# Performance work log

Hardware: AMD Instinct MI355X
Metric: run time of the kernel (lower is better)

Reference implementation:

```python
import jax, jax.numpy as jnp
import numpy as np

BATCH, SEQ, D_DIM, H = 8, 4096, 256, 64


def _log_step_init(u, dmin=0.001, dmax=0.1):
    lg_dmin, lg_dmax = np.log(dmin), np.log(dmax)
    return u * (lg_dmax - lg_dmin) + lg_dmin


def _make_hippo_nplr(N):
    q = np.arange(N)
    hip = np.sqrt((2 * q[:, None] + 1) * (2 * q[None, :] + 1))
    hip = np.where(q[:, None] > q[None, :], hip, 0.0) + np.diag(q + 1.0)
    hip = -hip
    p = np.sqrt(q + 0.5)
    S = hip + np.outer(p, p)  # NPLR: A = S - p p^T
    lam, V = np.linalg.eig(S)
    P = V.conj().T @ p
    B = V.conj().T @ (np.sqrt(2.0) * p)
    return lam.astype(np.complex64), P.astype(np.complex64), B.astype(np.complex64)


def _ri(z):
    return np.stack([z.real, z.imag], axis=-1).astype(np.float32)


def _cx(p):
    return p[..., 0] + 1j * p[..., 1]


def setup_inputs() -> dict:
    key = jax.random.key(0)
    k1, k2, k3 = jax.random.split(key, 3)
    lam, P, B = _make_hippo_nplr(H)
    lam_ri = jnp.asarray(_ri(lam))                      # (H, 2)
    P_ri = jnp.asarray(_ri(P))                          # (H, 2)
    B_ri = jnp.asarray(np.tile(_ri(B)[None], (D_DIM, 1, 1)))  # (D, H, 2)
    C_ri = jax.random.uniform(k1, (D_DIM, H, 2), dtype=jnp.float32)  # torch.rand complex
    Dp = jnp.ones((1, 1, D_DIM), dtype=jnp.float32)
    log_delta = jnp.asarray(
        _log_step_init(np.asarray(jax.random.uniform(k2, (D_DIM,), dtype=jnp.float32)))
    ).astype(jnp.float32)
    x = jax.random.normal(k3, (BATCH, SEQ, D_DIM), dtype=jnp.float32)
    return {"x": x, "lam_ri": lam_ri, "P_ri": P_ri, "B_ri": B_ri,
            "C_ri": C_ri, "D": Dp, "log_delta": log_delta}


def reference(x, lam_ri, P_ri, B_ri, C_ri, D, log_delta):
    # S4 DPLR generating-function kernel via Woodbury / Cauchy dot-products + iFFT conv.
    lam, P, B, C = _cx(lam_ri), _cx(P_ri), _cx(B_ri), _cx(C_ri)  # (H,), (H,), (D,H), (D,H)
    delta = jnp.exp(log_delta)                                   # (D,)
    L = x.shape[1]
    z = jnp.exp(2j * jnp.pi * jnp.arange(L) / L).astype(jnp.complex64)  # roots of unity (L,)
    coef = 2.0 / (1.0 + z)                                        # (L,)
    g = (2.0 * (1.0 - z) / (1.0 + z))[None, :] / delta[:, None].astype(jnp.complex64)  # (D, L)
    cauchy = 1.0 / (g[:, :, None] - lam[None, None, :])           # (D, L, H) -- R(z) diagonal
    # Woodbury: C (R - R P P* R / (1 + P* R P)) B  as 4 Cauchy dot products
    k00 = jnp.einsum("dh,dlh->dl", C * B, cauchy)
    k01 = jnp.einsum("dh,dlh->dl", C * P[None, :], cauchy)
    k10 = jnp.einsum("dh,dlh->dl", P.conj()[None, :] * B, cauchy)
    k11 = jnp.einsum("h,dlh->dl", P.conj() * P, cauchy)
    at_roots = coef[None, :] * (k00 - k01 * k10 / (1.0 + k11))    # (D, L)
    K = jnp.fft.ifft(at_roots, axis=-1).real.astype(x.dtype)      # (D, L) time-domain kernel
    # circular convolution along the sequence axis, per channel
    Xf = jnp.fft.fft(x, axis=1)                                   # (B, L, D)
    Kf = jnp.fft.fft(K, axis=-1)                                  # (D, L)
    y = jnp.fft.ifft(Xf * Kf.T[None, :, :], axis=1).real.astype(x.dtype)
    return y + D * x
```

## Files before the change

kernel.cpp:

```cpp
#include <hip/hip_runtime.h>
#include <math.h>

#ifndef M_PI
#define M_PI 3.14159265358979323846
#endif

#define BB 8
#define LL 4096
#define DD 256
#define HH 64

__device__ __forceinline__ float2 cmulf(float2 a, float2 b) {
    return make_float2(a.x*b.x - a.y*b.y, a.x*b.y + a.y*b.x);
}
__device__ __forceinline__ float2 cmul_cs(float2 a, float c, float s) {
    return make_float2(a.x*c - a.y*s, a.x*s + a.y*c);
}
__device__ __forceinline__ float2 cadd(float2 a, float2 b){return make_float2(a.x+b.x, a.y+b.y);}
__device__ __forceinline__ float2 csub(float2 a, float2 b){return make_float2(a.x-b.x, a.y-b.y);}

#define DR4(i) ((((i)&3)<<2)|((i)>>2))
#define SPW(k) ((((k)>>4)*17) + ((k)&15))

template<int SGN>
__device__ __forceinline__ void r4(float2& a, float2& b, float2& c, float2& d) {
    float2 e0 = cadd(a, c), e1 = csub(a, c);
    float2 o0 = cadd(b, d), o1 = csub(b, d);
    float2 j1 = (SGN < 0) ? make_float2(o1.y, -o1.x) : make_float2(-o1.y, o1.x);
    a = cadd(e0, o0);
    b = cadd(e1, j1);
    c = csub(e0, o0);
    d = csub(e1, j1);
}

template<int SGN>
__device__ __forceinline__ void fft16(float2 v[16]) {
    const float C16[10] = {1.f, 0.92387953f, 0.70710678f, 0.38268343f, 0.f,
                           -0.38268343f, -0.70710678f, -0.92387953f, -1.f, -0.92387953f};
    const float S16[10] = {0.f, 0.38268343f, 0.70710678f, 0.92387953f, 1.f,
                           0.92387953f, 0.70710678f, 0.38268343f, 0.f, -0.38268343f};
#pragma unroll
    for (int a0 = 0; a0 < 4; ++a0)
        r4<SGN>(v[a0], v[a0+4], v[a0+8], v[a0+12]);
#pragma unroll
    for (int a0 = 1; a0 < 4; ++a0) {
#pragma unroll
        for (int j0 = 1; j0 < 4; ++j0) {
            const int e = a0*j0;
            const float cc = C16[e];
            const float ss = (SGN < 0) ? -S16[e] : S16[e];
            v[a0 + 4*j0] = cmul_cs(v[a0 + 4*j0], cc, ss);
        }
    }
#pragma unroll
    for (int j0 = 0; j0 < 4; ++j0)
        r4<SGN>(v[4*j0+0], v[4*j0+1], v[4*j0+2], v[4*j0+3]);
}

__device__ __forceinline__ float2 woodbury_coef(
    float k00r, float k00i, float k01r, float k01i,
    float k10r, float k10i, float k11r, float k11i, float tc)
{
    float wr = 1.f + k11r, wi = k11i;
    float winv = __builtin_amdgcn_rcpf(wr*wr + wi*wi);
    float qr = k01r*k10r - k01i*k10i;
    float qi = k01r*k10i + k01i*k10r;
    float dr = (qr*wr + qi*wi) * winv;
    float di = (qi*wr - qr*wi) * winv;
    float rr = k00r - dr, ri = k00i - di;
    return make_float2(rr - tc*ri, tc*rr + ri);
}

__global__ __launch_bounds__(256)
void s4_cauchy_kf(const float* __restrict__ lam_ri,
                  const float* __restrict__ P_ri,
                  const float* __restrict__ B_ri,
                  const float* __restrict__ C_ri,
                  const float* __restrict__ Dp,
                  const float* __restrict__ log_delta,
                  float2* __restrict__ Kf)
{
    __shared__ float4 WA[HH];
    __shared__ float4 WB[HH];
    __shared__ float  WC[HH];
    const int d   = blockIdx.y;
    const int tid = threadIdx.x;
    if (tid < HH) {
        const int h = tid;
        float br = B_ri[(d*HH + h)*2 + 0], bi = B_ri[(d*HH + h)*2 + 1];
        float cr = C_ri[(d*HH + h)*2 + 0], ci = C_ri[(d*HH + h)*2 + 1];
        float pr = P_ri[h*2 + 0], pi = P_ri[h*2 + 1];
        WA[h] = make_float4(cr*br - ci*bi, cr*bi + ci*br,
                            cr*pr - ci*pi, cr*pi + ci*pr);
        WB[h] = make_float4(pr*br + pi*bi, pr*bi - pi*br,
                            pr*pr + pi*pi, -lam_ri[h*2+0]);
        WC[h] = lam_ri[h*2+1];
    }
    __syncthreads();
    const int t0 = blockIdx.x * blockDim.x + tid;
    const float delta = expf(log_delta[d]);
    const float dterm = Dp[d];
    const float SCALE = 0.5f / 4096.f;

    const int l1 = t0;
    const int l2 = t0 + 1024;

    float sn1, cs1, sn2, cs2;
    sincosf((float)l1 * (float)(M_PI/4096.0), &sn1, &cs1);
    sincosf((float)l2 * (float)(M_PI/4096.0), &sn2, &cs2);
    const float invd = __builtin_amdgcn_rcpf(delta);
    const float tt1 = sn1 * __builtin_amdgcn_rcpf(cs1);
    const float tt2 = sn2 * __builtin_amdgcn_rcpf(cs2);
    const float G1 = -2.f * tt1 * invd;
    const float G2 = -2.f * tt2 * invd;

    float a00r1=0,a00i1=0,a01r1=0,a01i1=0,a10r1=0,a10i1=0,a11r1=0,a11i1=0;
    float b00r1=0,b00i1=0,b01r1=0,b01i1=0;
    float a00r2=0,a00i2=0,a01r2=0,a01i2=0,a10r2=0,a10i2=0,a11r2=0,a11i2=0;
    float b00r2=0,b00i2=0,b01r2=0,b01i2=0;
    float sr2048 = 0.f;

#pragma unroll 4
    for (int h = 0; h < HH; ++h) {
        const float4 wa = WA[h];
        const float4 wb = WB[h];
        const float  li = WC[h];
        const float  nr  = wb.w;
        const float  nr2 = nr*nr;
        sr2048 += wa.x;
        {
            const float nip = G1 - li, nim = G1 + li;
            const float dp = fmaf(nip, nip, nr2);
            const float dm = fmaf(nim, nim, nr2);
            const float ip = __builtin_amdgcn_rcpf(dp*dm);
            const float invp = dm*ip, invm = dp*ip;
            const float rrp = nr*invp, rip = -nip*invp;
            const float rrm = nr*invm, rim =  nim*invm;
            a00r1 += wa.x*rrp - wa.y*rip;  a00i1 += wa.x*rip + wa.y*rrp;
            a01r1 += wa.z*rrp - wa.w*rip;  a01i1 += wa.z*rip + wa.w*rrp;
            a10r1 += wb.x*rrp - wb.y*rip;  a10i1 += wb.x*rip + wb.y*rrp;
            a11r1 += wb.z*rrp;             a11i1 += wb.z*rip;
            b00r1 += wa.x*rrm - wa.y*rim;  b00i1 += wa.x*rim + wa.y*rrm;
            b01r1 += wa.z*rrm - wa.w*rim;  b01i1 += wa.z*rim + wa.w*rrm;
        }
        {
            const float nip = G2 - li, nim = G2 + li;
            const float dp = fmaf(nip, nip, nr2);
            const float dm = fmaf(nim, nim, nr2);
            const float ip = __builtin_amdgcn_rcpf(dp*dm);
            const float invp = dm*ip, invm = dp*ip;
            const float rrp = nr*invp, rip = -nip*invp;
            const float rrm = nr*invm, rim =  nim*invm;
            a00r2 += wa.x*rrp - wa.y*rip;  a00i2 += wa.x*rip + wa.y*rrp;
            a01r2 += wa.z*rrp - wa.w*rip;  a01i2 += wa.z*rip + wa.w*rrp;
            a10r2 += wb.x*rrp - wb.y*rip;  a10i2 += wb.x*rip + wb.y*rrp;
            a11r2 += wb.z*rrp;             a11i2 += wb.z*rip;
            b00r2 += wa.x*rrm - wa.y*rim;  b00i2 += wa.x*rim + wa.y*rrm;
            b01r2 += wa.z*rrm - wa.w*rim;  b01i2 += wa.z*rim + wa.w*rrm;
        }
    }

    {
        float2 ar1 = woodbury_coef(a00r1,a00i1,a01r1,a01i1,a10r1,a10i1,a11r1,a11i1, -tt1);
        float2 ar2 = woodbury_coef(b00r1,b00i1,b01r1,b01i1,a10r1,-a10i1,a11r1,-a11i1, +tt1);
        float2 kf = make_float2((0.5f*(ar1.x + ar2.x) + dterm)*SCALE,
                                (0.5f*(ar1.y - ar2.y))*SCALE);
        Kf[(size_t)d*LL + l1] = kf;
    }
    {
        float2 ar1 = woodbury_coef(a00r2,a00i2,a01r2,a01i2,a10r2,a10i2,a11r2,a11i2, -tt2);
        float2 ar2 = woodbury_coef(b00r2,b00i2,b01r2,b01i2,a10r2,-a10i2,a11r2,-a11i2, +tt2);
        float2 kf = make_float2((0.5f*(ar1.x + ar2.x) + dterm)*SCALE,
                                (0.5f*(ar1.y - ar2.y))*SCALE);
        Kf[(size_t)d*LL + l2] = kf;
    }
    if (t0 == 0) {
        Kf[(size_t)d*LL + 2048] = make_float2((0.5f*delta*sr2048 + dterm)*SCALE, 0.f);
    }
}

__global__ __launch_bounds__(256)
void s4_fftconv(const float* __restrict__ x, const float2* __restrict__ Kf,
                float* __restrict__ y)
{
    __shared__ float2 As[4352];
    const int tid = threadIdx.x;
    const int p  = ((blockIdx.x & 7) << 7) | (blockIdx.x >> 3);
    const int b  = p >> 7;
    const int d2 = p & 127;

    const float2* xp = (const float2*)x + ((size_t)b*LL)*(DD/2) + d2;
    float2*       yp = (float2*)y       + ((size_t)b*LL)*(DD/2) + d2;
    const float2* Keb = Kf + (size_t)(2*d2)  *LL;
    const float2* Kob = Kf + (size_t)(2*d2+1)*LL;

    float2 v[16];

    {
        const int r = tid;
#pragma unroll
        for (int a = 0; a < 16; ++a)
            v[a] = xp[(size_t)(a*256 + r)*(DD/2)];
    }
    float2 pKe[9], pKo[9];
#pragma unroll
    for (int i = 0; i < 9; ++i) {
        int k = tid + (i << 8); if (k > 2048) k = 2048;
        pKe[i] = Keb[k];
        pKo[i] = Kob[k];
    }

    {
        const int r = tid;
        fft16<-1>(v);
        float2 base; sincosf(-(float)(2.0*M_PI/4096.0)*(float)r, &base.y, &base.x);
        float2 w = make_float2(1.f, 0.f);
#pragma unroll
        for (int k0 = 0; k0 < 16; ++k0) {
            As[17*r + k0] = cmulf(v[DR4(k0)], w);
            w = cmulf(w, base);
        }
    }
    __syncthreads();

    {
        const int k0 = tid >> 4, c = tid & 15;
#pragma unroll
        for (int bb = 0; bb < 16; ++bb)
            v[bb] = As[272*bb + 17*c + k0];
        __syncthreads();
        fft16<-1>(v);
        float2 base; sincosf(-(float)(2.0*M_PI/256.0)*(float)c, &base.y, &base.x);
        float2 w = make_float2(1.f, 0.f);
#pragma unroll
        for (int m0 = 0; m0 < 16; ++m0) {
            As[272*k0 + 17*c + m0] = cmulf(v[DR4(m0)], w);
            w = cmulf(w, base);
        }
    }
    __syncthreads();

    {
        const int k0 = tid >> 4, m0 = tid & 15;
#pragma unroll
        for (int c = 0; c < 16; ++c)
            v[c] = As[272*k0 + 17*c + m0];
        __syncthreads();
        fft16<-1>(v);
        const int s17 = 17*m0 + k0;
#pragma unroll
        for (int m1 = 0; m1 < 16; ++m1)
            As[s17 + 272*m1] = v[DR4(m1)];
    }
    __syncthreads();

    {
#pragma unroll
        for (int i = 0; i < 9; ++i) {
            int k = tid + (i << 8);
            if (k <= 2048) {
                int mk = (4096 - k) & 4095;
                float2 Zk = As[SPW(k)];
                float2 Zm = As[SPW(mk)];
                float2 Ke = pKe[i];
                float2 Ko = pKo[i];
                float2 S  = make_float2(Ke.x + Ko.x, Ke.y + Ko.y);
                float2 Df = make_float2(Ke.x - Ko.x, Ke.y - Ko.y);
                float2 cZm = make_float2(Zm.x, -Zm.y);
                float2 t0 = cmulf(Zk,  S);
                float2 t1 = cmulf(cZm, Df);
                float2 t2 = cmulf(cZm, S);
                float2 t3 = cmulf(Zk,  Df);
                As[SPW(k)]  = make_float2(t0.x + t1.x,   t0.y + t1.y);
                As[SPW(mk)] = make_float2(t2.x + t3.x, -(t2.y + t3.y));
            }
        }
    }
    __syncthreads();

    {
        const int k0 = tid >> 4, m0 = tid & 15;
        const int s17 = 17*m0 + k0;
#pragma unroll
        for (int m1 = 0; m1 < 16; ++m1)
            v[m1] = As[s17 + 272*m1];
        __syncthreads();
        fft16<1>(v);
        float2 base; sincosf((float)(2.0*M_PI/256.0)*(float)m0, &base.y, &base.x);
        float2 w = make_float2(1.f, 0.f);
#pragma unroll
        for (int c = 0; c < 16; ++c) {
            As[272*k0 + 17*c + m0] = cmulf(v[DR4(c)], w);
            w = cmulf(w, base);
        }
    }
    __syncthreads();

    {
        const int k0 = tid >> 4, c = tid & 15;
#pragma unroll
        for (int m0 = 0; m0 < 16; ++m0)
            v[m0] = As[272*k0 + 17*c + m0];
        __syncthreads();
        fft16<1>(v);
        float2 w, st;
        sincosf((float)(2.0*M_PI/4096.0)*(float)(c*k0), &w.y, &w.x);
        sincosf((float)(2.0*M_PI/256.0)*(float)k0,      &st.y, &st.x);
#pragma unroll
        for (int bb = 0; bb < 16; ++bb) {
            As[272*bb + 17*c + k0] = cmulf(v[DR4(bb)], w);
            w = cmulf(w, st);
        }
    }
    __syncthreads();

    {
        const int r = tid;
#pragma unroll
        for (int k0 = 0; k0 < 16; ++k0)
            v[k0] = As[17*r + k0];
        fft16<1>(v);
#pragma unroll
        for (int a = 0; a < 16; ++a)
            yp[(size_t)(a*256 + r)*(DD/2)] = v[DR4(a)];
    }
}

extern "C" void kernel_launch(void* const* d_in, const int* in_sizes, int n_in,
                              void* d_out, int out_size, void* d_ws, size_t ws_size,
                              hipStream_t stream)
{
    (void)in_sizes; (void)n_in; (void)out_size; (void)ws_size;
    const float* x         = (const float*)d_in[0];
    const float* lam_ri    = (const float*)d_in[1];
    const float* P_ri      = (const float*)d_in[2];
    const float* B_ri      = (const float*)d_in[3];
    const float* C_ri      = (const float*)d_in[4];
    const float* Dp        = (const float*)d_in[5];
    const float* log_delta = (const float*)d_in[6];
    float* y = (float*)d_out;

    float2* Kf = (float2*)d_ws;

    s4_cauchy_kf<<<dim3(4, DD), 256, 0, stream>>>(lam_ri, P_ri, B_ri, C_ri, Dp, log_delta, Kf);
    s4_fftconv<<<dim3(BB*DD/2), 256, 0, stream>>>(x, Kf, y);
}
```

Before: 163.9 us.

## Process four channels per block with float4 IO and XOR-swizzled shared memory

```diff
diff --git a/kernel.cpp b/kernel.cpp
--- a/kernel.cpp
+++ b/kernel.cpp
@@ -20,7 +20,7 @@
 __device__ __forceinline__ float2 csub(float2 a, float2 b){return make_float2(a.x-b.x, a.y-b.y);}
 
 #define DR4(i) ((((i)&3)<<2)|((i)>>2))
-#define SPW(k) ((((k)>>4)*17) + ((k)&15))
+#define LIDX(r,c) (((r)<<4) + (((c) ^ ((r)&15))))
 
 template<int SGN>
 __device__ __forceinline__ void r4(float2& a, float2& b, float2& c, float2& d) {
@@ -183,41 +183,38 @@
 void s4_fftconv(const float* __restrict__ x, const float2* __restrict__ Kf,
                 float* __restrict__ y)
 {
-    __shared__ float2 As[4352];
+    __shared__ float2 As[2][4096];
     const int tid = threadIdx.x;
-    const int p  = ((blockIdx.x & 7) << 7) | (blockIdx.x >> 3);
-    const int b  = p >> 7;
-    const int d2 = p & 127;
-
-    const float2* xp = (const float2*)x + ((size_t)b*LL)*(DD/2) + d2;
-    float2*       yp = (float2*)y       + ((size_t)b*LL)*(DD/2) + d2;
-    const float2* Keb = Kf + (size_t)(2*d2)  *LL;
-    const float2* Kob = Kf + (size_t)(2*d2+1)*LL;
-
-    float2 v[16];
+    const int p  = ((blockIdx.x & 7) << 6) | (blockIdx.x >> 3);
+    const int b  = p >> 6;
+    const int d4 = p & 63;
+
+    const float4* xq = (const float4*)x + ((size_t)b*LL)*(DD/4) + d4;
+    float4*       yq = (float4*)y       + ((size_t)b*LL)*(DD/4) + d4;
+    const float2* KeA = Kf + (size_t)(4*d4 + 0)*LL;
+    const float2* KoA = Kf + (size_t)(4*d4 + 1)*LL;
+    const float2* KeB = Kf + (size_t)(4*d4 + 2)*LL;
+    const float2* KoB = Kf + (size_t)(4*d4 + 3)*LL;
+
+    float2 vA[16], vB[16];
 
     {
         const int r = tid;
 #pragma unroll
-        for (int a = 0; a < 16; ++a)
-            v[a] = xp[(size_t)(a*256 + r)*(DD/2)];
-    }
-    float2 pKe[9], pKo[9];
-#pragma unroll
-    for (int i = 0; i < 9; ++i) {
-        int k = tid + (i << 8); if (k > 2048) k = 2048;
-        pKe[i] = Keb[k];
-        pKo[i] = Kob[k];
-    }
-
-    {
-        const int r = tid;
-        fft16<-1>(v);
+        for (int a = 0; a < 16; ++a) {
+            float4 f = xq[(size_t)(a*256 + r)*(DD/4)];
+            vA[a] = make_float2(f.x, f.y);
+            vB[a] = make_float2(f.z, f.w);
+        }
+        fft16<-1>(vA);
+        fft16<-1>(vB);
         float2 base; sincosf(-(float)(2.0*M_PI/4096.0)*(float)r, &base.y, &base.x);
         float2 w = make_float2(1.f, 0.f);
 #pragma unroll
         for (int k0 = 0; k0 < 16; ++k0) {
-            As[17*r + k0] = cmulf(v[DR4(k0)], w);
+            const int a0 = LIDX(r, k0);
+            As[0][a0] = cmulf(vA[DR4(k0)], w);
+            As[1][a0] = cmulf(vB[DR4(k0)], w);
             w = cmulf(w, base);
         }
     }
@@ -226,15 +223,21 @@
     {
         const int k0 = tid >> 4, c = tid & 15;
 #pragma unroll
-        for (int bb = 0; bb < 16; ++bb)
-            v[bb] = As[272*bb + 17*c + k0];
+        for (int bb = 0; bb < 16; ++bb) {
+            const int a0 = LIDX(16*bb + c, k0);
+            vA[bb] = As[0][a0];
+            vB[bb] = As[1][a0];
+        }
         __syncthreads();
-        fft16<-1>(v);
+        fft16<-1>(vA);
+        fft16<-1>(vB);
         float2 base; sincosf(-(float)(2.0*M_PI/256.0)*(float)c, &base.y, &base.x);
         float2 w = make_float2(1.f, 0.f);
 #pragma unroll
         for (int m0 = 0; m0 < 16; ++m0) {
-            As[272*k0 + 17*c + m0] = cmulf(v[DR4(m0)], w);
+            const int a0 = LIDX(16*k0 + c, m0);
+            As[0][a0] = cmulf(vA[DR4(m0)], w);
+            As[1][a0] = cmulf(vB[DR4(m0)], w);
             w = cmulf(w, base);
         }
     }
@@ -243,14 +246,20 @@
     {
         const int k0 = tid >> 4, m0 = tid & 15;
 #pragma unroll
-        for (int c = 0; c < 16; ++c)
-            v[c] = As[272*k0 + 17*c + m0];
+        for (int c = 0; c < 16; ++c) {
+            const int a0 = LIDX(16*k0 + c, m0);
+            vA[c] = As[0][a0];
+            vB[c] = As[1][a0];
+        }
         __syncthreads();
-        fft16<-1>(v);
-        const int s17 = 17*m0 + k0;
-#pragma unroll
-        for (int m1 = 0; m1 < 16; ++m1)
-            As[s17 + 272*m1] = v[DR4(m1)];
+        fft16<-1>(vA);
+        fft16<-1>(vB);
+#pragma unroll
+        for (int m1 = 0; m1 < 16; ++m1) {
+            const int a0 = LIDX(m0 + 16*m1, k0);
+            As[0][a0] = vA[DR4(m1)];
+            As[1][a0] = vB[DR4(m1)];
+        }
     }
     __syncthreads();
 
@@ -259,20 +268,35 @@
         for (int i = 0; i < 9; ++i) {
             int k = tid + (i << 8);
             if (k <= 2048) {
-                int mk = (4096 - k) & 4095;
-                float2 Zk = As[SPW(k)];
-                float2 Zm = As[SPW(mk)];
-                float2 Ke = pKe[i];
-                float2 Ko = pKo[i];
-                float2 S  = make_float2(Ke.x + Ko.x, Ke.y + Ko.y);
-                float2 Df = make_float2(Ke.x - Ko.x, Ke.y - Ko.y);
-                float2 cZm = make_float2(Zm.x, -Zm.y);
-                float2 t0 = cmulf(Zk,  S);
-                float2 t1 = cmulf(cZm, Df);
-                float2 t2 = cmulf(cZm, S);
-                float2 t3 = cmulf(Zk,  Df);
-                As[SPW(k)]  = make_float2(t0.x + t1.x,   t0.y + t1.y);
-                As[SPW(mk)] = make_float2(t2.x + t3.x, -(t2.y + t3.y));
+                const int mk = (4096 - k) & 4095;
+                const int ak = LIDX(k>>4,  k&15);
+                const int am = LIDX(mk>>4, mk&15);
+                {
+                    float2 Zk = As[0][ak], Zm = As[0][am];
+                    float2 Ke = KeA[k],    Ko = KoA[k];
+                    float2 S  = make_float2(Ke.x + Ko.x, Ke.y + Ko.y);
+                    float2 Df = make_float2(Ke.x - Ko.x, Ke.y - Ko.y);
+                    float2 cZm = make_float2(Zm.x, -Zm.y);
+                    float2 t0 = cmulf(Zk,  S);
+                    float2 t1 = cmulf(cZm, Df);
+                    float2 t2 = cmulf(cZm, S);
+                    float2 t3 = cmulf(Zk,  Df);
+                    As[0][ak] = make_float2(t0.x + t1.x,   t0.y + t1.y);
+                    As[0][am] = make_float2(t2.x + t3.x, -(t2.y + t3.y));
+                }
+                {
+                    float2 Zk = As[1][ak], Zm = As[1][am];
+                    float2 Ke = KeB[k],    Ko = KoB[k];
+                    float2 S  = make_float2(Ke.x + Ko.x, Ke.y + Ko.y);
+                    float2 Df = make_float2(Ke.x - Ko.x, Ke.y - Ko.y);
+                    float2 cZm = make_float2(Zm.x, -Zm.y);
+                    float2 t0 = cmulf(Zk,  S);
+                    float2 t1 = cmulf(cZm, Df);
+                    float2 t2 = cmulf(cZm, S);
+                    float2 t3 = cmulf(Zk,  Df);
+                    As[1][ak] = make_float2(t0.x + t1.x,   t0.y + t1.y);
+                    As[1][am] = make_float2(t2.x + t3.x, -(t2.y + t3.y));
+                }
             }
         }
     }
@@ -280,17 +304,22 @@
 
     {
         const int k0 = tid >> 4, m0 = tid & 15;
-        const int s17 = 17*m0 + k0;
-#pragma unroll
-        for (int m1 = 0; m1 < 16; ++m1)
-            v[m1] = As[s17 + 272*m1];
+#pragma unroll
+        for (int m1 = 0; m1 < 16; ++m1) {
+            const int a0 = LIDX(m0 + 16*m1, k0);
+            vA[m1] = As[0][a0];
+            vB[m1] = As[1][a0];
+        }
         __syncthreads();
-        fft16<1>(v);
+        fft16<1>(vA);
+        fft16<1>(vB);
         float2 base; sincosf((float)(2.0*M_PI/256.0)*(float)m0, &base.y, &base.x);
         float2 w = make_float2(1.f, 0.f);
 #pragma unroll
         for (int c = 0; c < 16; ++c) {
-            As[272*k0 + 17*c + m0] = cmulf(v[DR4(c)], w);
+            const int a0 = LIDX(16*k0 + c, m0);
+            As[0][a0] = cmulf(vA[DR4(c)], w);
+            As[1][a0] = cmulf(vB[DR4(c)], w);
             w = cmulf(w, base);
         }
     }
@@ -299,16 +328,22 @@
     {
         const int k0 = tid >> 4, c = tid & 15;
 #pragma unroll
-        for (int m0 = 0; m0 < 16; ++m0)
-            v[m0] = As[272*k0 + 17*c + m0];
+        for (int m0 = 0; m0 < 16; ++m0) {
+            const int a0 = LIDX(16*k0 + c, m0);
+            vA[m0] = As[0][a0];
+            vB[m0] = As[1][a0];
+        }
         __syncthreads();
-        fft16<1>(v);
+        fft16<1>(vA);
+        fft16<1>(vB);
         float2 w, st;
         sincosf((float)(2.0*M_PI/4096.0)*(float)(c*k0), &w.y, &w.x);
         sincosf((float)(2.0*M_PI/256.0)*(float)k0,      &st.y, &st.x);
 #pragma unroll
         for (int bb = 0; bb < 16; ++bb) {
-            As[272*bb + 17*c + k0] = cmulf(v[DR4(bb)], w);
+            const int a0 = LIDX(16*bb + c, k0);
+            As[0][a0] = cmulf(vA[DR4(bb)], w);
+            As[1][a0] = cmulf(vB[DR4(bb)], w);
             w = cmulf(w, st);
         }
     }
@@ -317,12 +352,18 @@
     {
         const int r = tid;
 #pragma unroll
-        for (int k0 = 0; k0 < 16; ++k0)
-            v[k0] = As[17*r + k0];
-        fft16<1>(v);
-#pragma unroll
-        for (int a = 0; a < 16; ++a)
-            yp[(size_t)(a*256 + r)*(DD/2)] = v[DR4(a)];
+        for (int k0 = 0; k0 < 16; ++k0) {
+            const int a0 = LIDX(r, k0);
+            vA[k0] = As[0][a0];
+            vB[k0] = As[1][a0];
+        }
+        fft16<1>(vA);
+        fft16<1>(vB);
+#pragma unroll
+        for (int a = 0; a < 16; ++a) {
+            float2 oa = vA[DR4(a)], ob = vB[DR4(a)];
+            yq[(size_t)(a*256 + r)*(DD/4)] = make_float4(oa.x, oa.y, ob.x, ob.y);
+        }
     }
 }
 
@@ -343,5 +384,5 @@
     float2* Kf = (float2*)d_ws;
 
     s4_cauchy_kf<<<dim3(4, DD), 256, 0, stream>>>(lam_ri, P_ri, B_ri, C_ri, Dp, log_delta, Kf);
-    s4_fftconv<<<dim3(BB*DD/2), 256, 0, stream>>>(x, Kf, y);
-}
+    s4_fftconv<<<dim3(BB*DD/4), 256, 0, stream>>>(x, Kf, y);
+}
```

New measurement: 157.9 us. 3.7% less time.
